# Kernel optimization log

Hardware: AMD Instinct MI355X
Metric: run time of the kernel (lower is better)

Reference implementation:

```python
import jax, jax.numpy as jnp
import numpy as np

B, N, DIM = 4, 2048, 512
HEADS, DIM_HEAD = 8, 64
HID = HEADS * DIM_HEAD


def setup_inputs() -> dict:
    key = jax.random.key(0)
    k1, k2, k3, k4, k5 = jax.random.split(key, 5)
    x = jax.random.normal(k1, (B, N, DIM), jnp.float32)
    pos_bias = jax.random.normal(k2, (HEADS, N, N), jnp.float32) * 0.02
    focus_present_mask = jax.random.bernoulli(k3, 0.5, (B,))
    w_qkv = jax.random.normal(k4, (DIM, 3 * HID), jnp.float32) * (DIM ** -0.5)
    w_out = jax.random.normal(k5, (HID, DIM), jnp.float32) * (HID ** -0.5)
    return {"x": x, "pos_bias": pos_bias, "focus_present_mask": focus_present_mask,
            "w_qkv": w_qkv, "w_out": w_out}


def reference(x, pos_bias, focus_present_mask, w_qkv, w_out):
    scale = DIM_HEAD ** -0.5
    qkv = x @ w_qkv                                   # (B, N, 3*HID)
    q, k, v = jnp.split(qkv, 3, axis=-1)

    def to_heads(t):  # (B, N, HID) -> (B, H, N, D)
        return t.reshape(B, N, HEADS, DIM_HEAD).transpose(0, 2, 1, 3)

    q = to_heads(q) * scale
    k = to_heads(k)
    v = to_heads(v)

    sim = jnp.einsum('bhid,bhjd->bhij', q, k) + pos_bias[None]  # (B, H, N, N)

    # focus_present_mask[b] True -> attend only to self (eye); False -> attend all
    eye = jnp.eye(N, dtype=bool)
    mask = jnp.where(focus_present_mask[:, None, None, None],
                     eye[None, None], jnp.bool_(True))          # (B,1,N,N)
    sim = jnp.where(mask, sim, -jnp.finfo(sim.dtype).max)

    attn = jax.nn.softmax(sim, axis=-1)  # stable softmax == subtract-max + softmax
    out = jnp.einsum('bhij,bhjd->bhid', attn, v)
    out = out.transpose(0, 2, 1, 3).reshape(B, N, HID)
    return out @ w_out
```

## Files before the change

### kernel.cpp

```cpp
#include <hip/hip_runtime.h>
#include <hip/hip_bf16.h>
#include <float.h>

#define B_   4
#define N_   2048
#define DIM_ 512
#define H_   8
#define DH_  64

typedef unsigned short ushort;
typedef __attribute__((ext_vector_type(8))) short short8;
typedef __attribute__((ext_vector_type(4))) float f32x4;

__device__ __forceinline__ ushort f2bf(float f) {
    union { float f; unsigned u; } v; v.f = f;
    return (ushort)((v.u + 0x7fffu + ((v.u >> 16) & 1u)) >> 16);
}
__device__ __forceinline__ float bf2f(ushort u) {
    union { unsigned u; float f; } v; v.u = ((unsigned)u) << 16;
    return v.f;
}

typedef const __attribute__((address_space(1))) unsigned int* gas_t;
typedef __attribute__((address_space(3))) unsigned int* las_t;
__device__ __forceinline__ void gl_lds16(const void* g, void* l) {
    __builtin_amdgcn_global_load_lds((gas_t)g, (las_t)l, 16, 0, 0);
}

__global__ __launch_bounds__(256) void prep_kernel(
    const float* __restrict__ x, const float* __restrict__ wqkv,
    const float* __restrict__ wo,
    ushort* __restrict__ xb, ushort* __restrict__ wqkvT, ushort* __restrict__ woT)
{
    __shared__ ushort tile[64][72];
    const int bx = blockIdx.x;
    const int t = threadIdx.x;
    if (bx < 2048) {
        int gid = bx * 256 + t;
        const float4* xv = (const float4*)x;
        float4 v0 = xv[gid * 2], v1 = xv[gid * 2 + 1];
        uint4 pk;
        pk.x = (unsigned)f2bf(v0.x) | ((unsigned)f2bf(v0.y) << 16);
        pk.y = (unsigned)f2bf(v0.z) | ((unsigned)f2bf(v0.w) << 16);
        pk.z = (unsigned)f2bf(v1.x) | ((unsigned)f2bf(v1.y) << 16);
        pk.w = (unsigned)f2bf(v1.z) | ((unsigned)f2bf(v1.w) << 16);
        ((uint4*)xb)[gid] = pk;
        return;
    }
    int bi = bx - 2048;
    const float* src; ushort* dst; int C, tc, tr;
    if (bi < 192) { src = wqkv; dst = wqkvT; C = 1536; tc = bi % 24; tr = bi / 24; }
    else { bi -= 192; src = wo; dst = woT; C = 512; tc = bi & 7; tr = bi >> 3; }

    const int row = t >> 2, c16 = (t & 3) * 16;
    const float* sp = src + (size_t)(tr * 64 + row) * C + tc * 64 + c16;
    #pragma unroll
    for (int i = 0; i < 4; ++i) {
        float4 v = ((const float4*)sp)[i];
        tile[row][c16 + i * 4 + 0] = f2bf(v.x);
        tile[row][c16 + i * 4 + 1] = f2bf(v.y);
        tile[row][c16 + i * 4 + 2] = f2bf(v.z);
        tile[row][c16 + i * 4 + 3] = f2bf(v.w);
    }
    __syncthreads();
    ushort s[16];
    #pragma unroll
    for (int i = 0; i < 16; ++i) s[i] = tile[c16 + i][row];
    ushort* dp = dst + (size_t)(tc * 64 + row) * 512 + tr * 64 + c16;
    *(uint4*)dp       = *(uint4*)&s[0];
    *(uint4*)(dp + 8) = *(uint4*)&s[8];
}

__global__ __launch_bounds__(256) void vtrans_kernel(
    const ushort* __restrict__ v, ushort* __restrict__ vT)
{
    __shared__ ushort tile[64][72];
    const int nt = blockIdx.x, bh = blockIdx.y;
    const int t = threadIdx.x;
    const int row = t >> 2, c16 = (t & 3) * 16;
    const ushort* src = v + ((size_t)bh * 2048 + nt * 64 + row) * 64 + c16;
    *(uint4*)&tile[row][c16]     = *(const uint4*)src;
    *(uint4*)&tile[row][c16 + 8] = *(const uint4*)(src + 8);
    __syncthreads();
    ushort s[16];
    #pragma unroll
    for (int i = 0; i < 16; ++i) s[i] = tile[c16 + i][row];
    ushort* dst = vT + ((size_t)bh * 64 + row) * 2048 + nt * 64 + c16;
    *(uint4*)dst       = *(uint4*)&s[0];
    *(uint4*)(dst + 8) = *(uint4*)&s[8];
}

__global__ __launch_bounds__(256) void qkv_gemm(
    const ushort* __restrict__ A, const ushort* __restrict__ Bt,
    ushort* __restrict__ qb, ushort* __restrict__ kb, ushort* __restrict__ vb)
{
    __shared__ ushort sA[128 * 64];
    __shared__ ushort sB[128 * 64];
    const int bn = blockIdx.x;
    const int bm = blockIdx.y;
    const int t = threadIdx.x, w_id = t >> 6, lane = t & 63;
    const int l15 = lane & 15, quad = lane >> 4;
    const int mo = (w_id & 1) * 64, no = (w_id >> 1) * 64;
    const int lr = lane >> 3, lc = (lane & 7) * 8;

    f32x4 acc[4][4] = {};

    for (int kt = 0; kt < 8; ++kt) {
        __syncthreads();
        #pragma unroll
        for (int i = 0; i < 4; ++i) {
            int j = w_id * 4 + i;
            gl_lds16(A  + (size_t)(bm * 128 + j * 8 + lr) * 512 + kt * 64 + lc, &sA[j * 512]);
            gl_lds16(Bt + (size_t)(bn * 128 + j * 8 + lr) * 512 + kt * 64 + lc, &sB[j * 512]);
        }
        __syncthreads();
        #pragma unroll
        for (int c = 0; c < 2; ++c) {
            short8 af[4], bf[4];
            #pragma unroll
            for (int mt = 0; mt < 4; ++mt)
                af[mt] = *(const short8*)&sA[(mo + mt * 16 + l15) * 64 + c * 32 + quad * 8];
            #pragma unroll
            for (int n2 = 0; n2 < 4; ++n2)
                bf[n2] = *(const short8*)&sB[(no + n2 * 16 + l15) * 64 + c * 32 + quad * 8];
            #pragma unroll
            for (int mt = 0; mt < 4; ++mt)
                #pragma unroll
                for (int n2 = 0; n2 < 4; ++n2)
                    acc[mt][n2] = __builtin_amdgcn_mfma_f32_16x16x32_bf16(af[mt], bf[n2], acc[mt][n2], 0, 0, 0);
        }
    }

    const int gn0 = bn * 128 + no;
    const int which = gn0 >> 9;
    const int h = (gn0 >> 6) & 7;
    ushort* dst = which == 0 ? qb : (which == 1 ? kb : vb);
    const float sc = which == 0 ? 0.125f : 1.0f;
    #pragma unroll
    for (int mt = 0; mt < 4; ++mt) {
        const int m0 = bm * 128 + mo + mt * 16 + quad * 4;
        #pragma unroll
        for (int n2 = 0; n2 < 4; ++n2) {
            int d = n2 * 16 + l15;
            #pragma unroll
            for (int r = 0; r < 4; ++r) {
                int m = m0 + r, b = m >> 11, n = m & 2047;
                dst[((size_t)(b * 8 + h) * 2048 + n) * 64 + d] = f2bf(acc[mt][n2][r] * sc);
            }
        }
    }
}

__global__ __launch_bounds__(256) void attn_kernel(
    const ushort* __restrict__ qg, const ushort* __restrict__ kg,
    const ushort* __restrict__ vTg, const float* __restrict__ bias,
    const int* __restrict__ mask,
    ushort* __restrict__ po, float* __restrict__ pl)
{
    const int bid = blockIdx.x;
    const int qblk = bid & 31, s = (bid >> 5) & 1, h = (bid >> 6) & 7, b = bid >> 9;
    if (mask[b] != 0) return;

    const int t = threadIdx.x, w_id = t >> 6, lane = t & 63;
    const int l15 = lane & 15, quad = lane >> 4;
    const int lr = lane >> 3, lc = (lane & 7) * 8;
    const int bh = b * 8 + h;
    const int kbase = s * 1024;

    __shared__ ushort lds_k[64 * 64];
    __shared__ ushort lds_vt[64 * 64];
    __shared__ ushort lds_sp[4 * 16 * 68];

    const ushort* kptr = kg  + (size_t)bh * 2048 * 64;
    const ushort* vtp  = vTg + (size_t)bh * 64 * 2048;

    const ushort* qrp = qg + (size_t)bh * 2048 * 64 + (size_t)(qblk * 64 + w_id * 16 + l15) * 64;
    short8 qf0 = *(const short8*)(qrp + quad * 8);
    short8 qf1 = *(const short8*)(qrp + 32 + quad * 8);

    const int qrow0 = qblk * 64 + w_id * 16 + quad * 4;
    const float* bp = bias + ((size_t)h * 2048 + qrow0) * 2048 + kbase;

    float breg[16];
    #pragma unroll
    for (int tt = 0; tt < 4; ++tt)
        #pragma unroll
        for (int r = 0; r < 4; ++r)
            breg[tt * 4 + r] = bp[(size_t)r * 2048 + tt * 16 + l15];

    f32x4 o[4] = {};
    float lsum[4] = {0.f, 0.f, 0.f, 0.f};

    for (int it = 0; it < 16; ++it) {
        __syncthreads();
        #pragma unroll
        for (int i = 0; i < 2; ++i) {
            int j = w_id * 2 + i;
            gl_lds16(kptr + (size_t)(kbase + it * 64 + j * 8 + lr) * 64 + lc, &lds_k[j * 512]);
            gl_lds16(vtp + (size_t)(j * 8 + lr) * 2048 + kbase + it * 64 + lc, &lds_vt[j * 512]);
        }
        __syncthreads();

        f32x4 sv[4] = {};
        #pragma unroll
        for (int tt = 0; tt < 4; ++tt) {
            short8 kf0 = *(const short8*)&lds_k[(tt * 16 + l15) * 64 + quad * 8];
            short8 kf1 = *(const short8*)&lds_k[(tt * 16 + l15) * 64 + 32 + quad * 8];
            sv[tt] = __builtin_amdgcn_mfma_f32_16x16x32_bf16(qf0, kf0, sv[tt], 0, 0, 0);
            sv[tt] = __builtin_amdgcn_mfma_f32_16x16x32_bf16(qf1, kf1, sv[tt], 0, 0, 0);
        }
        #pragma unroll
        for (int tt = 0; tt < 4; ++tt)
            #pragma unroll
            for (int r = 0; r < 4; ++r)
                sv[tt][r] += breg[tt * 4 + r];

        if (it < 15) {
            #pragma unroll
            for (int tt = 0; tt < 4; ++tt)
                #pragma unroll
                for (int r = 0; r < 4; ++r)
                    breg[tt * 4 + r] = bp[(size_t)r * 2048 + (it + 1) * 64 + tt * 16 + l15];
        }

        const int prow0 = (w_id * 16 + quad * 4) * 68;
        #pragma unroll
        for (int r = 0; r < 4; ++r) {
            float e0 = __expf(sv[0][r]), e1 = __expf(sv[1][r]);
            float e2 = __expf(sv[2][r]), e3 = __expf(sv[3][r]);
            lsum[r] += (e0 + e1) + (e2 + e3);
            const int pr = prow0 + r * 68;
            lds_sp[pr + l15]      = f2bf(e0);
            lds_sp[pr + 16 + l15] = f2bf(e1);
            lds_sp[pr + 32 + l15] = f2bf(e2);
            lds_sp[pr + 48 + l15] = f2bf(e3);
        }

        asm volatile("s_waitcnt lgkmcnt(0)" ::: "memory");

        short8 pf0 = *(const short8*)&lds_sp[(w_id * 16 + l15) * 68 + quad * 8];
        short8 pf1 = *(const short8*)&lds_sp[(w_id * 16 + l15) * 68 + 32 + quad * 8];
        #pragma unroll
        for (int nt = 0; nt < 4; ++nt) {
            short8 vf0 = *(const short8*)&lds_vt[(nt * 16 + l15) * 64 + quad * 8];
            short8 vf1 = *(const short8*)&lds_vt[(nt * 16 + l15) * 64 + 32 + quad * 8];
            o[nt] = __builtin_amdgcn_mfma_f32_16x16x32_bf16(pf0, vf0, o[nt], 0, 0, 0);
            o[nt] = __builtin_amdgcn_mfma_f32_16x16x32_bf16(pf1, vf1, o[nt], 0, 0, 0);
        }
    }

    #pragma unroll
    for (int r = 0; r < 4; ++r) {
        #pragma unroll
        for (int off = 1; off < 16; off <<= 1)
            lsum[r] += __shfl_xor(lsum[r], off, 64);
    }

    #pragma unroll
    for (int r = 0; r < 4; ++r) {
        const int qrow = qrow0 + r;
        const size_t base = ((size_t)(s * 32 + bh) * 2048 + qrow) * 64;
        #pragma unroll
        for (int nt = 0; nt < 4; ++nt)
            po[base + nt * 16 + l15] = f2bf(o[nt][r]);
        if (l15 == 0)
            pl[(size_t)(s * 32 + bh) * 2048 + qrow] = lsum[r];
    }
}

__global__ __launch_bounds__(256) void combine_kernel(
    const ushort* __restrict__ po, const float* __restrict__ pl,
    const ushort* __restrict__ vb, const int* __restrict__ mask,
    ushort* __restrict__ ob)
{
    const int gid = blockIdx.x * 256 + threadIdx.x;
    const int dd = (gid & 7) * 8;
    const int h = (gid >> 3) & 7, n = (gid >> 6) & 2047, b = gid >> 17;
    const int bh = b * 8 + h;
    ushort* op = ob + ((size_t)b * 2048 + n) * 512 + h * 64 + dd;
    if (mask[b] != 0) {
        *(uint4*)op = *(const uint4*)(vb + ((size_t)bh * 2048 + n) * 64 + dd);
        return;
    }
    const size_t i1 = (size_t)bh * 2048 + n;
    const size_t i2 = (size_t)(32 + bh) * 2048 + n;
    float inv = 1.f / (pl[i1] + pl[i2]);
    uint4 ua = *(const uint4*)(po + i1 * 64 + dd);
    uint4 ub = *(const uint4*)(po + i2 * 64 + dd);
    const ushort* pa = (const ushort*)&ua;
    const ushort* pb = (const ushort*)&ub;
    ushort res[8];
    #pragma unroll
    for (int j = 0; j < 8; ++j)
        res[j] = f2bf((bf2f(pa[j]) + bf2f(pb[j])) * inv);
    *(uint4*)op = *(uint4*)res;
}

__global__ __launch_bounds__(256) void out_gemm(
    const ushort* __restrict__ A, const ushort* __restrict__ Bt,
    float* __restrict__ out)
{
    __shared__ ushort sA[128 * 64];
    __shared__ ushort sB[128 * 64];
    const int bn = blockIdx.x;
    const int bm = blockIdx.y;
    const int t = threadIdx.x, w_id = t >> 6, lane = t & 63;
    const int l15 = lane & 15, quad = lane >> 4;
    const int mo = (w_id & 1) * 64, no = (w_id >> 1) * 64;
    const int lr = lane >> 3, lc = (lane & 7) * 8;

    f32x4 acc[4][4] = {};

    for (int kt = 0; kt < 8; ++kt) {
        __syncthreads();
        #pragma unroll
        for (int i = 0; i < 4; ++i) {
            int j = w_id * 4 + i;
            gl_lds16(A  + (size_t)(bm * 128 + j * 8 + lr) * 512 + kt * 64 + lc, &sA[j * 512]);
            gl_lds16(Bt + (size_t)(bn * 128 + j * 8 + lr) * 512 + kt * 64 + lc, &sB[j * 512]);
        }
        __syncthreads();
        #pragma unroll
        for (int c = 0; c < 2; ++c) {
            short8 af[4], bf[4];
            #pragma unroll
            for (int mt = 0; mt < 4; ++mt)
                af[mt] = *(const short8*)&sA[(mo + mt * 16 + l15) * 64 + c * 32 + quad * 8];
            #pragma unroll
            for (int n2 = 0; n2 < 4; ++n2)
                bf[n2] = *(const short8*)&sB[(no + n2 * 16 + l15) * 64 + c * 32 + quad * 8];
            #pragma unroll
            for (int mt = 0; mt < 4; ++mt)
                #pragma unroll
                for (int n2 = 0; n2 < 4; ++n2)
                    acc[mt][n2] = __builtin_amdgcn_mfma_f32_16x16x32_bf16(af[mt], bf[n2], acc[mt][n2], 0, 0, 0);
        }
    }
    #pragma unroll
    for (int mt = 0; mt < 4; ++mt) {
        const int m0 = bm * 128 + mo + mt * 16 + quad * 4;
        #pragma unroll
        for (int n2 = 0; n2 < 4; ++n2) {
            int col = bn * 128 + no + n2 * 16 + l15;
            #pragma unroll
            for (int r = 0; r < 4; ++r)
                out[(size_t)(m0 + r) * 512 + col] = acc[mt][n2][r];
        }
    }
}

extern "C" void kernel_launch(void* const* d_in, const int* in_sizes, int n_in,
                              void* d_out, int out_size, void* d_ws, size_t ws_size,
                              hipStream_t stream)
{
    const float* x        = (const float*)d_in[0];
    const float* pos_bias = (const float*)d_in[1];
    const int*   mask     = (const int*)d_in[2];
    const float* w_qkv    = (const float*)d_in[3];
    const float* w_out    = (const float*)d_in[4];
    float* out = (float*)d_out;

    char* ws = (char*)d_ws;
    ushort* qb    = (ushort*)(ws + 0);
    ushort* kb    = (ushort*)(ws + 8388608);
    ushort* vb    = (ushort*)(ws + 16777216);
    ushort* vT    = (ushort*)(ws + 25165824);
    ushort* xb    = (ushort*)(ws + 33554432);
    ushort* ob    = (ushort*)(ws + 33554432);
    ushort* po    = (ushort*)(ws + 41943040);
    float*  pl    = (float* )(ws + 58720256);
    ushort* woT   = (ushort*)(ws + 59244544);
    ushort* wqkvT = (ushort*)(ws + 59768832);

    prep_kernel<<<2304, 256, 0, stream>>>(x, w_qkv, w_out, xb, wqkvT, woT);
    qkv_gemm<<<dim3(12, 64), 256, 0, stream>>>(xb, wqkvT, qb, kb, vb);
    vtrans_kernel<<<dim3(32, 32), 256, 0, stream>>>(vb, vT);
    attn_kernel<<<2048, 256, 0, stream>>>(qb, kb, vT, pos_bias, mask, po, pl);
    combine_kernel<<<2048, 256, 0, stream>>>(po, pl, vb, mask, ob);
    out_gemm<<<dim3(4, 64), 256, 0, stream>>>(ob, woT, out);
}
```

Before: 299.3 us.

## Double-buffer K/V and GEMM tiles with XOR-swizzled LDS layouts

Adds double-buffered LDS tiles to the attention kernel and the output GEMM, so the next K/V (or A/B) tile is prefetched by direct global-to-LDS loads while the current tile is computed. This leaves one barrier per iteration instead of two. LDS rows are XOR-swizzled (and the P scratch is unpadded but swizzled) to avoid bank conflicts, V fragments are loaded early, and s_setprio raises wave priority around MFMA blocks. The doubled LDS use and the launch-bounds occupancy hint may lower occupancy or add register pressure.

```diff
diff --git a/kernel.cpp b/kernel.cpp
--- a/kernel.cpp
+++ b/kernel.cpp
@@ -151,7 +151,7 @@
     }
 }
 
-__global__ __launch_bounds__(256) void attn_kernel(
+__global__ __launch_bounds__(256, 4) void attn_kernel(
     const ushort* __restrict__ qg, const ushort* __restrict__ kg,
     const ushort* __restrict__ vTg, const float* __restrict__ bias,
     const int* __restrict__ mask,
@@ -163,16 +163,25 @@
 
     const int t = threadIdx.x, w_id = t >> 6, lane = t & 63;
     const int l15 = lane & 15, quad = lane >> 4;
-    const int lr = lane >> 3, lc = (lane & 7) * 8;
+    const int lr = lane >> 3;
+    const int lcs = ((lane & 7) ^ lr) * 8;
+    const int rsw = l15 & 7;
     const int bh = b * 8 + h;
     const int kbase = s * 1024;
 
-    __shared__ ushort lds_k[64 * 64];
-    __shared__ ushort lds_vt[64 * 64];
-    __shared__ ushort lds_sp[4 * 16 * 68];
+    __shared__ ushort lds_k[2][64 * 64];
+    __shared__ ushort lds_vt[2][64 * 64];
+    __shared__ ushort lds_sp[4 * 16 * 64];
 
     const ushort* kptr = kg  + (size_t)bh * 2048 * 64;
     const ushort* vtp  = vTg + (size_t)bh * 64 * 2048;
+
+    #pragma unroll
+    for (int i = 0; i < 2; ++i) {
+        int j = w_id * 2 + i;
+        gl_lds16(kptr + (size_t)(kbase + j * 8 + lr) * 64 + lcs, &lds_k[0][j * 512]);
+        gl_lds16(vtp + (size_t)(j * 8 + lr) * 2048 + kbase + lcs, &lds_vt[0][j * 512]);
+    }
 
     const ushort* qrp = qg + (size_t)bh * 2048 * 64 + (size_t)(qblk * 64 + w_id * 16 + l15) * 64;
     short8 qf0 = *(const short8*)(qrp + quad * 8);
@@ -191,24 +200,45 @@
     f32x4 o[4] = {};
     float lsum[4] = {0.f, 0.f, 0.f, 0.f};
 
+    asm volatile("s_waitcnt vmcnt(0)" ::: "memory");
+    __syncthreads();
+
     for (int it = 0; it < 16; ++it) {
-        __syncthreads();
-        #pragma unroll
-        for (int i = 0; i < 2; ++i) {
-            int j = w_id * 2 + i;
-            gl_lds16(kptr + (size_t)(kbase + it * 64 + j * 8 + lr) * 64 + lc, &lds_k[j * 512]);
-            gl_lds16(vtp + (size_t)(j * 8 + lr) * 2048 + kbase + it * 64 + lc, &lds_vt[j * 512]);
-        }
-        __syncthreads();
+        const int cur = it & 1;
+        const ushort* lk = lds_k[cur];
+        const ushort* lv = lds_vt[cur];
+
+        if (it + 1 < 16) {
+            #pragma unroll
+            for (int i = 0; i < 2; ++i) {
+                int j = w_id * 2 + i;
+                gl_lds16(kptr + (size_t)(kbase + (it + 1) * 64 + j * 8 + lr) * 64 + lcs,
+                         &lds_k[cur ^ 1][j * 512]);
+                gl_lds16(vtp + (size_t)(j * 8 + lr) * 2048 + kbase + (it + 1) * 64 + lcs,
+                         &lds_vt[cur ^ 1][j * 512]);
+            }
+        }
 
         f32x4 sv[4] = {};
+        __builtin_amdgcn_s_setprio(1);
         #pragma unroll
         for (int tt = 0; tt < 4; ++tt) {
-            short8 kf0 = *(const short8*)&lds_k[(tt * 16 + l15) * 64 + quad * 8];
-            short8 kf1 = *(const short8*)&lds_k[(tt * 16 + l15) * 64 + 32 + quad * 8];
+            const ushort* kr = &lk[(tt * 16 + l15) * 64];
+            short8 kf0 = *(const short8*)&kr[(quad ^ rsw) * 8];
+            short8 kf1 = *(const short8*)&kr[((4 + quad) ^ rsw) * 8];
             sv[tt] = __builtin_amdgcn_mfma_f32_16x16x32_bf16(qf0, kf0, sv[tt], 0, 0, 0);
             sv[tt] = __builtin_amdgcn_mfma_f32_16x16x32_bf16(qf1, kf1, sv[tt], 0, 0, 0);
         }
+        __builtin_amdgcn_s_setprio(0);
+
+        short8 vfa[4], vfb[4];
+        #pragma unroll
+        for (int nt = 0; nt < 4; ++nt) {
+            const ushort* vr = &lv[(nt * 16 + l15) * 64];
+            vfa[nt] = *(const short8*)&vr[(quad ^ rsw) * 8];
+            vfb[nt] = *(const short8*)&vr[((4 + quad) ^ rsw) * 8];
+        }
+
         #pragma unroll
         for (int tt = 0; tt < 4; ++tt)
             #pragma unroll
@@ -223,30 +253,37 @@
                     breg[tt * 4 + r] = bp[(size_t)r * 2048 + (it + 1) * 64 + tt * 16 + l15];
         }
 
-        const int prow0 = (w_id * 16 + quad * 4) * 68;
         #pragma unroll
         for (int r = 0; r < 4; ++r) {
             float e0 = __expf(sv[0][r]), e1 = __expf(sv[1][r]);
             float e2 = __expf(sv[2][r]), e3 = __expf(sv[3][r]);
             lsum[r] += (e0 + e1) + (e2 + e3);
-            const int pr = prow0 + r * 68;
-            lds_sp[pr + l15]      = f2bf(e0);
-            lds_sp[pr + 16 + l15] = f2bf(e1);
-            lds_sp[pr + 32 + l15] = f2bf(e2);
-            lds_sp[pr + 48 + l15] = f2bf(e3);
+            const int prow = w_id * 16 + quad * 4 + r;
+            const int prs = prow & 7;
+            const int ch = l15 >> 3;
+            ushort* pb = &lds_sp[prow * 64 + (l15 & 7)];
+            pb[((0 + ch) ^ prs) * 8] = f2bf(e0);
+            pb[((2 + ch) ^ prs) * 8] = f2bf(e1);
+            pb[((4 + ch) ^ prs) * 8] = f2bf(e2);
+            pb[((6 + ch) ^ prs) * 8] = f2bf(e3);
         }
 
         asm volatile("s_waitcnt lgkmcnt(0)" ::: "memory");
-
-        short8 pf0 = *(const short8*)&lds_sp[(w_id * 16 + l15) * 68 + quad * 8];
-        short8 pf1 = *(const short8*)&lds_sp[(w_id * 16 + l15) * 68 + 32 + quad * 8];
+        __builtin_amdgcn_sched_barrier(0);
+
+        const ushort* sp = &lds_sp[(w_id * 16 + l15) * 64];
+        short8 pf0 = *(const short8*)&sp[(quad ^ rsw) * 8];
+        short8 pf1 = *(const short8*)&sp[((4 + quad) ^ rsw) * 8];
+        __builtin_amdgcn_s_setprio(1);
         #pragma unroll
         for (int nt = 0; nt < 4; ++nt) {
-            short8 vf0 = *(const short8*)&lds_vt[(nt * 16 + l15) * 64 + quad * 8];
-            short8 vf1 = *(const short8*)&lds_vt[(nt * 16 + l15) * 64 + 32 + quad * 8];
-            o[nt] = __builtin_amdgcn_mfma_f32_16x16x32_bf16(pf0, vf0, o[nt], 0, 0, 0);
-            o[nt] = __builtin_amdgcn_mfma_f32_16x16x32_bf16(pf1, vf1, o[nt], 0, 0, 0);
-        }
+            o[nt] = __builtin_amdgcn_mfma_f32_16x16x32_bf16(pf0, vfa[nt], o[nt], 0, 0, 0);
+            o[nt] = __builtin_amdgcn_mfma_f32_16x16x32_bf16(pf1, vfb[nt], o[nt], 0, 0, 0);
+        }
+        __builtin_amdgcn_s_setprio(0);
+
+        asm volatile("s_waitcnt vmcnt(0)" ::: "memory");
+        __syncthreads();
     }
 
     #pragma unroll
@@ -300,41 +337,59 @@
     const ushort* __restrict__ A, const ushort* __restrict__ Bt,
     float* __restrict__ out)
 {
-    __shared__ ushort sA[128 * 64];
-    __shared__ ushort sB[128 * 64];
+    __shared__ ushort sA[2][128 * 64];
+    __shared__ ushort sB[2][128 * 64];
     const int bn = blockIdx.x;
     const int bm = blockIdx.y;
     const int t = threadIdx.x, w_id = t >> 6, lane = t & 63;
     const int l15 = lane & 15, quad = lane >> 4;
     const int mo = (w_id & 1) * 64, no = (w_id >> 1) * 64;
-    const int lr = lane >> 3, lc = (lane & 7) * 8;
+    const int lr = lane >> 3;
+    const int lcs = ((lane & 7) ^ lr) * 8;
+    const int rsw = l15 & 7;
 
     f32x4 acc[4][4] = {};
 
+    #pragma unroll
+    for (int i = 0; i < 4; ++i) {
+        int j = w_id * 4 + i;
+        gl_lds16(A  + (size_t)(bm * 128 + j * 8 + lr) * 512 + lcs, &sA[0][j * 512]);
+        gl_lds16(Bt + (size_t)(bn * 128 + j * 8 + lr) * 512 + lcs, &sB[0][j * 512]);
+    }
+    asm volatile("s_waitcnt vmcnt(0)" ::: "memory");
+    __syncthreads();
+
     for (int kt = 0; kt < 8; ++kt) {
-        __syncthreads();
-        #pragma unroll
-        for (int i = 0; i < 4; ++i) {
-            int j = w_id * 4 + i;
-            gl_lds16(A  + (size_t)(bm * 128 + j * 8 + lr) * 512 + kt * 64 + lc, &sA[j * 512]);
-            gl_lds16(Bt + (size_t)(bn * 128 + j * 8 + lr) * 512 + kt * 64 + lc, &sB[j * 512]);
-        }
-        __syncthreads();
+        const int cur = kt & 1;
+        if (kt + 1 < 8) {
+            #pragma unroll
+            for (int i = 0; i < 4; ++i) {
+                int j = w_id * 4 + i;
+                gl_lds16(A  + (size_t)(bm * 128 + j * 8 + lr) * 512 + (kt + 1) * 64 + lcs,
+                         &sA[cur ^ 1][j * 512]);
+                gl_lds16(Bt + (size_t)(bn * 128 + j * 8 + lr) * 512 + (kt + 1) * 64 + lcs,
+                         &sB[cur ^ 1][j * 512]);
+            }
+        }
         #pragma unroll
         for (int c = 0; c < 2; ++c) {
             short8 af[4], bf[4];
             #pragma unroll
             for (int mt = 0; mt < 4; ++mt)
-                af[mt] = *(const short8*)&sA[(mo + mt * 16 + l15) * 64 + c * 32 + quad * 8];
+                af[mt] = *(const short8*)&sA[cur][(mo + mt * 16 + l15) * 64 + (((c * 4 + quad) ^ rsw)) * 8];
             #pragma unroll
             for (int n2 = 0; n2 < 4; ++n2)
-                bf[n2] = *(const short8*)&sB[(no + n2 * 16 + l15) * 64 + c * 32 + quad * 8];
+                bf[n2] = *(const short8*)&sB[cur][(no + n2 * 16 + l15) * 64 + (((c * 4 + quad) ^ rsw)) * 8];
+            __builtin_amdgcn_s_setprio(1);
             #pragma unroll
             for (int mt = 0; mt < 4; ++mt)
                 #pragma unroll
                 for (int n2 = 0; n2 < 4; ++n2)
                     acc[mt][n2] = __builtin_amdgcn_mfma_f32_16x16x32_bf16(af[mt], bf[n2], acc[mt][n2], 0, 0, 0);
-        }
+            __builtin_amdgcn_s_setprio(0);
+        }
+        asm volatile("s_waitcnt vmcnt(0)" ::: "memory");
+        __syncthreads();
     }
     #pragma unroll
     for (int mt = 0; mt < 4; ++mt) {
```

Result: slower. 305.9 us (+2.2%).
